# Kernel tuning notes

Hardware: AMD Instinct MI355X
Metric: run time of the kernel (lower is better)

The kernel has to match this reference:

```python
import jax, jax.numpy as jnp
import numpy as np

HIDDEN_DIM = 128

def custom_softmax(x, axis):
    e = jnp.exp(x)
    e = jnp.where(jnp.isinf(e), jnp.float32(1e30), e)
    s = jnp.sum(e, axis=axis, keepdims=True)
    return e / (s + 1e-14)

def setup_inputs() -> dict:
    key = jax.random.key(0)
    k1, k2, k3, kq, kk, kv = jax.random.split(key, 6)
    B, L, D = 4, 4096, 256
    x1 = jax.random.normal(k1, (B, L, D), dtype=jnp.float32)
    x2 = jax.random.normal(k2, (B, L, D), dtype=jnp.float32)
    x3 = jax.random.normal(k3, (B, L, D), dtype=jnp.float32)
    mask = jnp.zeros((L, L), dtype=jnp.float32)
    # nn.Linear(D, H, bias=False): kaiming-uniform-ish init, stored as [D, H] for x @ W
    lim = 1.0 / np.sqrt(D)
    Wq = jax.random.uniform(kq, (D, HIDDEN_DIM), jnp.float32, -lim, lim)
    Wk = jax.random.uniform(kk, (D, HIDDEN_DIM), jnp.float32, -lim, lim)
    Wv = jax.random.uniform(kv, (D, HIDDEN_DIM), jnp.float32, -lim, lim)
    return {"x1": x1, "x2": x2, "x3": x3, "mask": mask, "Wq": Wq, "Wk": Wk, "Wv": Wv}

def reference(x1, x2, x3, mask, Wq, Wk, Wv):
    q = jnp.einsum('bld,dh->blh', x1, Wq)
    k = jnp.einsum('bld,dh->blh', x2, Wk)
    v = jnp.einsum('bld,dh->blh', x3, Wv)
    scale = 1.0 / jnp.sqrt(jnp.float32(HIDDEN_DIM))
    scores = jnp.einsum('bqh,bkh->bqk', q, k) * scale  # [B, L, L]
    weights = custom_softmax(scores + mask, axis=-1)
    return jnp.einsum('bqk,bkh->bqh', weights, v)
```

## Files before the change

### kernel.cpp

```cpp
#include <hip/hip_runtime.h>
#include <hip/hip_bf16.h>

typedef __attribute__((ext_vector_type(8))) short bf16x8;
typedef __attribute__((ext_vector_type(4))) float f32x4;

#define QSCALE 0.088388347648318447f

static __device__ __forceinline__ f32x4 mfma16(bf16x8 a, bf16x8 b, f32x4 c) {
    return __builtin_amdgcn_mfma_f32_16x16x32_bf16(a, b, c, 0, 0, 0);
}

union BF8 { bf16x8 v; __hip_bfloat16 b[8]; };

__global__ void wt_kernel(const float* __restrict__ Wq, const float* __restrict__ Wk,
                          const float* __restrict__ Wv, __hip_bfloat16* __restrict__ wt)
{
    const int w = blockIdx.y;
    const float* W = (w == 0) ? Wq : ((w == 1) ? Wk : Wv);
    const int e = blockIdx.x * 256 + threadIdx.x;
    const int h = e >> 8, d = e & 255;
    wt[w * 32768 + e] = __float2bfloat16(W[d * 128 + h]);
}

__global__ __launch_bounds__(256, 1) void proj_kernel(
    const float* __restrict__ x1, const float* __restrict__ x2, const float* __restrict__ x3,
    const __hip_bfloat16* __restrict__ wt,
    __hip_bfloat16* __restrict__ q_ws, __hip_bfloat16* __restrict__ k_ws,
    __hip_bfloat16* __restrict__ vt_ws)
{
    __shared__ __align__(16) __hip_bfloat16 t_lds[64 * 136];
    const int mode = blockIdx.y;
    const float* x = (mode == 0) ? x1 : ((mode == 1) ? x2 : x3);
    const __hip_bfloat16* wp = wt + mode * 32768;
    const int tid = threadIdx.x, wid = tid >> 6, lane = tid & 63;
    const int l15 = lane & 15, lhi = lane >> 4;
    const int m0 = blockIdx.x * 64 + wid * 16;

    bf16x8 xa[8];
    const float* xr = x + (size_t)(m0 + l15) * 256;
    #pragma unroll
    for (int ks = 0; ks < 8; ks++) {
        const int d0 = ks * 32 + lhi * 8;
        const float4 lo = *(const float4*)(xr + d0);
        const float4 hi = *(const float4*)(xr + d0 + 4);
        BF8 pk;
        pk.b[0] = __float2bfloat16(lo.x); pk.b[1] = __float2bfloat16(lo.y);
        pk.b[2] = __float2bfloat16(lo.z); pk.b[3] = __float2bfloat16(lo.w);
        pk.b[4] = __float2bfloat16(hi.x); pk.b[5] = __float2bfloat16(hi.y);
        pk.b[6] = __float2bfloat16(hi.z); pk.b[7] = __float2bfloat16(hi.w);
        xa[ks] = pk.v;
    }

    f32x4 acc[8];
    #pragma unroll
    for (int hg = 0; hg < 8; hg++) acc[hg] = (f32x4){0.f, 0.f, 0.f, 0.f};

    #pragma unroll
    for (int hg = 0; hg < 8; hg++) {
        #pragma unroll
        for (int ks = 0; ks < 8; ks++) {
            const bf16x8 wb = *(const bf16x8*)(wp + (hg * 16 + l15) * 256 + ks * 32 + lhi * 8);
            acc[hg] = mfma16(xa[ks], wb, acc[hg]);
        }
    }

    if (mode < 2) {
        __hip_bfloat16* outp = (mode == 0) ? q_ws : k_ws;
        const float osc = (mode == 0) ? QSCALE : 1.0f;
        #pragma unroll
        for (int hg = 0; hg < 8; hg++)
            #pragma unroll
            for (int r = 0; r < 4; r++)
                outp[(size_t)(m0 + lhi * 4 + r) * 128 + hg * 16 + l15] =
                    __float2bfloat16(acc[hg][r] * osc);
    } else {
        #pragma unroll
        for (int hg = 0; hg < 8; hg++)
            #pragma unroll
            for (int r = 0; r < 4; r++)
                t_lds[(wid * 16 + lhi * 4 + r) * 136 + hg * 16 + l15] =
                    __float2bfloat16(acc[hg][r]);
        __syncthreads();
        const int b  = (blockIdx.x * 64) >> 12;
        const int l0 = (blockIdx.x * 64) & 4095;
        const int h = tid >> 1, lh = (tid & 1) * 32;
        #pragma unroll
        for (int c = 0; c < 4; c++) {
            BF8 ov;
            #pragma unroll
            for (int j = 0; j < 8; j++) ov.b[j] = t_lds[(lh + c * 8 + j) * 136 + h];
            *(bf16x8*)(vt_ws + (size_t)(b * 128 + h) * 4096 + l0 + lh + c * 8) = ov.v;
        }
    }
}

__global__ __launch_bounds__(256, 1) void attn_kernel(
    const __hip_bfloat16* __restrict__ q_ws,
    const __hip_bfloat16* __restrict__ k_ws,
    const __hip_bfloat16* __restrict__ vt_ws,
    float* __restrict__ dst,
    float* __restrict__ l_ws,
    const int nsplit)
{
    __shared__ __align__(16) __hip_bfloat16 k_lds[64 * 128];
    __shared__ __align__(16) __hip_bfloat16 v_lds[128 * 64];
    __shared__ __align__(16) __hip_bfloat16 p_lds[4][32 * 64];

    const int tid = threadIdx.x, wid = tid >> 6, lane = tid & 63;
    const int l15 = lane & 15, lhi = lane >> 4;
    const int qt = blockIdx.x, b = blockIdx.y, half = blockIdx.z;
    const int q0 = qt * 128 + wid * 32;

    bf16x8 qa[2][4];
    #pragma unroll
    for (int s = 0; s < 2; s++)
        #pragma unroll
        for (int c = 0; c < 4; c++)
            qa[s][c] = *(const bf16x8*)(q_ws +
                (size_t)(b * 4096 + q0 + s * 16 + l15) * 128 + c * 32 + lhi * 8);

    f32x4 o[2][8];
    #pragma unroll
    for (int s = 0; s < 2; s++)
        #pragma unroll
        for (int hg = 0; hg < 8; hg++) o[s][hg] = (f32x4){0.f, 0.f, 0.f, 0.f};
    float rs[2][4] = {{0.f,0.f,0.f,0.f},{0.f,0.f,0.f,0.f}};

    const int ntile = (nsplit == 2) ? 32 : 64;
    const int kbase = half * 2048;

    for (int kt = 0; kt < ntile; kt++) {
        const int k0 = kbase + kt * 64;
        __syncthreads();
        #pragma unroll
        for (int p = 0; p < 4; p++) {
            const int key = (tid >> 4) + p * 16;
            const int cc = tid & 15;
            const bf16x8 kv = *(const bf16x8*)(k_ws + (size_t)(b * 4096 + k0 + key) * 128 + cc * 8);
            *(bf16x8*)&k_lds[key * 128 + (((cc >> 1) ^ (key & 7)) << 4) + ((cc & 1) << 3)] = kv;
        }
        #pragma unroll
        for (int p = 0; p < 4; p++) {
            const int h = (tid >> 3) + p * 32;
            const int cc = tid & 7;
            const bf16x8 vv = *(const bf16x8*)(vt_ws + (size_t)(b * 128 + h) * 4096 + k0 + cc * 8);
            *(bf16x8*)&v_lds[h * 64 + (((cc >> 1) ^ (h & 3)) << 4) + ((cc & 1) << 3)] = vv;
        }
        __syncthreads();

        #pragma unroll
        for (int kg = 0; kg < 4; kg++) {
            f32x4 s0 = (f32x4){0.f,0.f,0.f,0.f};
            f32x4 s1 = (f32x4){0.f,0.f,0.f,0.f};
            const int key = kg * 16 + l15;
            #pragma unroll
            for (int c = 0; c < 4; c++) {
                const int chunk = (c << 1) | (lhi >> 1);
                const bf16x8 kb = *(const bf16x8*)&k_lds[key * 128 +
                    ((chunk ^ (key & 7)) << 4) + ((lhi & 1) << 3)];
                s0 = mfma16(qa[0][c], kb, s0);
                s1 = mfma16(qa[1][c], kb, s1);
            }
            #pragma unroll
            for (int r = 0; r < 4; r++) {
                float e0 = __expf(s0[r]); e0 = fminf(e0, 1e30f);
                float e1 = __expf(s1[r]); e1 = fminf(e1, 1e30f);
                rs[0][r] += e0; rs[1][r] += e1;
                const int row0 = lhi * 4 + r;
                p_lds[wid][row0 * 64 + ((kg ^ lhi) << 4) + l15] = __float2bfloat16(e0);
                p_lds[wid][(row0 + 16) * 64 + ((kg ^ lhi) << 4) + l15] = __float2bfloat16(e1);
            }
        }

        bf16x8 pa[2][2];
        #pragma unroll
        for (int s = 0; s < 2; s++)
            #pragma unroll
            for (int ks = 0; ks < 2; ks++) {
                const int prow = s * 16 + l15;
                const int chunk = (ks << 1) | (lhi >> 1);
                pa[s][ks] = *(const bf16x8*)&p_lds[wid][prow * 64 +
                    ((chunk ^ (l15 >> 2)) << 4) + ((lhi & 1) << 3)];
            }

        #pragma unroll
        for (int hg = 0; hg < 8; hg++) {
            #pragma unroll
            for (int ks = 0; ks < 2; ks++) {
                const int h = hg * 16 + l15;
                const int chunk = (ks << 1) | (lhi >> 1);
                const bf16x8 vb = *(const bf16x8*)&v_lds[h * 64 +
                    ((chunk ^ (h & 3)) << 4) + ((lhi & 1) << 3)];
                o[0][hg] = mfma16(pa[0][ks], vb, o[0][hg]);
                o[1][hg] = mfma16(pa[1][ks], vb, o[1][hg]);
            }
        }
    }

    #pragma unroll
    for (int s = 0; s < 2; s++)
        #pragma unroll
        for (int r = 0; r < 4; r++) {
            float v = rs[s][r];
            v += __shfl_xor(v, 1);
            v += __shfl_xor(v, 2);
            v += __shfl_xor(v, 4);
            v += __shfl_xor(v, 8);
            rs[s][r] = v;
        }

    if (nsplit == 2) {
        const int bq = (half * 4 + b) * 4096 + q0;
        #pragma unroll
        for (int s = 0; s < 2; s++)
            #pragma unroll
            for (int r = 0; r < 4; r++)
                #pragma unroll
                for (int hg = 0; hg < 8; hg++)
                    dst[(size_t)(bq + s * 16 + lhi * 4 + r) * 128 + hg * 16 + l15] = o[s][hg][r];
        if (l15 == 0) {
            #pragma unroll
            for (int s = 0; s < 2; s++)
                #pragma unroll
                for (int r = 0; r < 4; r++)
                    l_ws[bq + s * 16 + lhi * 4 + r] = rs[s][r];
        }
    } else {
        const int bq = b * 4096 + q0;
        #pragma unroll
        for (int s = 0; s < 2; s++)
            #pragma unroll
            for (int r = 0; r < 4; r++) {
                const float inv = 1.0f / (rs[s][r] + 1e-14f);
                #pragma unroll
                for (int hg = 0; hg < 8; hg++)
                    dst[(size_t)(bq + s * 16 + lhi * 4 + r) * 128 + hg * 16 + l15] =
                        o[s][hg][r] * inv;
            }
    }
}

__global__ void combine_kernel(const float* __restrict__ num_ws, const float* __restrict__ l_ws,
                               float* __restrict__ out)
{
    const int idx = blockIdx.x * 256 + threadIdx.x;
    const int bq = idx >> 7;
    const float n = num_ws[idx] + num_ws[idx + 2097152];
    const float l = l_ws[bq] + l_ws[bq + 16384] + 1e-14f;
    out[idx] = n / l;
}

extern "C" void kernel_launch(void* const* d_in, const int* in_sizes, int n_in,
                              void* d_out, int out_size, void* d_ws, size_t ws_size,
                              hipStream_t stream)
{
    const float* x1 = (const float*)d_in[0];
    const float* x2 = (const float*)d_in[1];
    const float* x3 = (const float*)d_in[2];
    const float* Wq = (const float*)d_in[4];
    const float* Wk = (const float*)d_in[5];
    const float* Wv = (const float*)d_in[6];
    float* out = (float*)d_out;

    char* ws = (char*)d_ws;
    __hip_bfloat16* q_ws  = (__hip_bfloat16*)(ws + 0);
    __hip_bfloat16* k_ws  = (__hip_bfloat16*)(ws + (4u  << 20));
    __hip_bfloat16* vt_ws = (__hip_bfloat16*)(ws + (8u  << 20));
    __hip_bfloat16* wt_ws = (__hip_bfloat16*)(ws + (12u << 20));
    float* num_ws = (float*)(ws + (13u << 20));
    float* l_ws   = (float*)(ws + (29u << 20));

    const size_t need2 = (29ull << 20) + 131072ull;
    const int nsplit = (ws_size >= need2) ? 2 : 1;

    wt_kernel<<<dim3(128, 3), 256, 0, stream>>>(Wq, Wk, Wv, wt_ws);
    proj_kernel<<<dim3(256, 3), 256, 0, stream>>>(x1, x2, x3, wt_ws, q_ws, k_ws, vt_ws);
    if (nsplit == 2) {
        attn_kernel<<<dim3(32, 4, 2), 256, 0, stream>>>(q_ws, k_ws, vt_ws, num_ws, l_ws, 2);
        combine_kernel<<<8192, 256, 0, stream>>>(num_ws, l_ws, out);
    } else {
        attn_kernel<<<dim3(32, 4, 1), 256, 0, stream>>>(q_ws, k_ws, vt_ws, out, l_ws, 1);
    }
}
```

Before: 232.7 us.

## Split attention keys four ways, prefetch K/V tiles into registers, vectorize combine

```diff
diff --git a/kernel.cpp b/kernel.cpp
--- a/kernel.cpp
+++ b/kernel.cpp
@@ -22,7 +22,7 @@
     wt[w * 32768 + e] = __float2bfloat16(W[d * 128 + h]);
 }
 
-__global__ __launch_bounds__(256, 1) void proj_kernel(
+__global__ __launch_bounds__(256, 3) void proj_kernel(
     const float* __restrict__ x1, const float* __restrict__ x2, const float* __restrict__ x3,
     const __hip_bfloat16* __restrict__ wt,
     __hip_bfloat16* __restrict__ q_ws, __hip_bfloat16* __restrict__ k_ws,
@@ -108,7 +108,7 @@
 
     const int tid = threadIdx.x, wid = tid >> 6, lane = tid & 63;
     const int l15 = lane & 15, lhi = lane >> 4;
-    const int qt = blockIdx.x, b = blockIdx.y, half = blockIdx.z;
+    const int qt = blockIdx.x, b = blockIdx.y, sp = blockIdx.z;
     const int q0 = qt * 128 + wid * 32;
 
     bf16x8 qa[2][4];
@@ -126,26 +126,38 @@
         for (int hg = 0; hg < 8; hg++) o[s][hg] = (f32x4){0.f, 0.f, 0.f, 0.f};
     float rs[2][4] = {{0.f,0.f,0.f,0.f},{0.f,0.f,0.f,0.f}};
 
-    const int ntile = (nsplit == 2) ? 32 : 64;
-    const int kbase = half * 2048;
+    const int ntile = 64 / nsplit;
+    const int kbase = sp * (4096 / nsplit);
+
+    const int kkey = tid >> 4, kcc = tid & 15;
+    const int vh = tid >> 3, vcc = tid & 7;
+    const __hip_bfloat16* kbp = k_ws + (size_t)b * 4096 * 128;
+    const __hip_bfloat16* vbp = vt_ws + (size_t)b * 128 * 4096;
+
+    bf16x8 kpre[4], vpre[4];
+    auto issue = [&](int k0) {
+        #pragma unroll
+        for (int p = 0; p < 4; p++) {
+            kpre[p] = *(const bf16x8*)(kbp + (size_t)(k0 + kkey + p * 16) * 128 + kcc * 8);
+            vpre[p] = *(const bf16x8*)(vbp + (size_t)(vh + p * 32) * 4096 + k0 + vcc * 8);
+        }
+    };
+    auto commit = [&]() {
+        #pragma unroll
+        for (int p = 0; p < 4; p++) {
+            const int key = kkey + p * 16;
+            *(bf16x8*)&k_lds[key * 128 + (((kcc >> 1) ^ (key & 7)) << 4) + ((kcc & 1) << 3)] = kpre[p];
+            const int h = vh + p * 32;
+            *(bf16x8*)&v_lds[h * 64 + (((vcc >> 1) ^ (h & 3)) << 4) + ((vcc & 1) << 3)] = vpre[p];
+        }
+    };
+
+    issue(kbase);
 
     for (int kt = 0; kt < ntile; kt++) {
-        const int k0 = kbase + kt * 64;
         __syncthreads();
-        #pragma unroll
-        for (int p = 0; p < 4; p++) {
-            const int key = (tid >> 4) + p * 16;
-            const int cc = tid & 15;
-            const bf16x8 kv = *(const bf16x8*)(k_ws + (size_t)(b * 4096 + k0 + key) * 128 + cc * 8);
-            *(bf16x8*)&k_lds[key * 128 + (((cc >> 1) ^ (key & 7)) << 4) + ((cc & 1) << 3)] = kv;
-        }
-        #pragma unroll
-        for (int p = 0; p < 4; p++) {
-            const int h = (tid >> 3) + p * 32;
-            const int cc = tid & 7;
-            const bf16x8 vv = *(const bf16x8*)(vt_ws + (size_t)(b * 128 + h) * 4096 + k0 + cc * 8);
-            *(bf16x8*)&v_lds[h * 64 + (((cc >> 1) ^ (h & 3)) << 4) + ((cc & 1) << 3)] = vv;
-        }
+        commit();
+        if (kt + 1 < ntile) issue(kbase + (kt + 1) * 64);
         __syncthreads();
 
         #pragma unroll
@@ -209,8 +221,8 @@
             rs[s][r] = v;
         }
 
-    if (nsplit == 2) {
-        const int bq = (half * 4 + b) * 4096 + q0;
+    if (nsplit > 1) {
+        const int bq = (sp * 4 + b) * 4096 + q0;
         #pragma unroll
         for (int s = 0; s < 2; s++)
             #pragma unroll
@@ -240,14 +252,20 @@
     }
 }
 
-__global__ void combine_kernel(const float* __restrict__ num_ws, const float* __restrict__ l_ws,
-                               float* __restrict__ out)
+__global__ void combine_kernel(const float4* __restrict__ num_ws, const float* __restrict__ l_ws,
+                               float4* __restrict__ out, const int nsplit)
 {
     const int idx = blockIdx.x * 256 + threadIdx.x;
-    const int bq = idx >> 7;
-    const float n = num_ws[idx] + num_ws[idx + 2097152];
-    const float l = l_ws[bq] + l_ws[bq + 16384] + 1e-14f;
-    out[idx] = n / l;
+    const int bq = idx >> 5;
+    float4 n = {0.f, 0.f, 0.f, 0.f};
+    float l = 1e-14f;
+    for (int s = 0; s < nsplit; s++) {
+        const float4 t = num_ws[idx + s * 524288];
+        n.x += t.x; n.y += t.y; n.z += t.z; n.w += t.w;
+        l += l_ws[bq + s * 16384];
+    }
+    const float inv = 1.0f / l;
+    out[idx] = (float4){n.x * inv, n.y * inv, n.z * inv, n.w * inv};
 }
 
 extern "C" void kernel_launch(void* const* d_in, const int* in_sizes, int n_in,
@@ -268,16 +286,21 @@
     __hip_bfloat16* vt_ws = (__hip_bfloat16*)(ws + (8u  << 20));
     __hip_bfloat16* wt_ws = (__hip_bfloat16*)(ws + (12u << 20));
     float* num_ws = (float*)(ws + (13u << 20));
-    float* l_ws   = (float*)(ws + (29u << 20));
-
-    const size_t need2 = (29ull << 20) + 131072ull;
-    const int nsplit = (ws_size >= need2) ? 2 : 1;
+    const size_t num_bytes4 = 4ull * (8u << 20);
+    const size_t num_bytes2 = 2ull * (8u << 20);
+
+    int nsplit = 1;
+    size_t l_off;
+    if (ws_size >= (13u << 20) + num_bytes4 + (1u << 20)) { nsplit = 4; l_off = (13u << 20) + num_bytes4; }
+    else if (ws_size >= (13u << 20) + num_bytes2 + (1u << 20)) { nsplit = 2; l_off = (13u << 20) + num_bytes2; }
+    else { l_off = (13u << 20); }
+    float* l_ws = (float*)(ws + l_off);
 
     wt_kernel<<<dim3(128, 3), 256, 0, stream>>>(Wq, Wk, Wv, wt_ws);
     proj_kernel<<<dim3(256, 3), 256, 0, stream>>>(x1, x2, x3, wt_ws, q_ws, k_ws, vt_ws);
-    if (nsplit == 2) {
-        attn_kernel<<<dim3(32, 4, 2), 256, 0, stream>>>(q_ws, k_ws, vt_ws, num_ws, l_ws, 2);
-        combine_kernel<<<8192, 256, 0, stream>>>(num_ws, l_ws, out);
+    if (nsplit > 1) {
+        attn_kernel<<<dim3(32, 4, nsplit), 256, 0, stream>>>(q_ws, k_ws, vt_ws, num_ws, l_ws, nsplit);
+        combine_kernel<<<2048, 256, 0, stream>>>((const float4*)num_ws, l_ws, (float4*)out, nsplit);
     } else {
         attn_kernel<<<dim3(32, 4, 1), 256, 0, stream>>>(q_ws, k_ws, vt_ws, out, l_ws, 1);
     }
```

Result: faster. 212.3 us (-8.8%).
